# Kernel tuning notes

Hardware: AMD Instinct MI355X
Metric: run time of the kernel (lower is better)

## Reference

```python
import jax, jax.numpy as jnp
import numpy as np

QUALITY = 95
X_MIN, X_MAX = 0.0, 1.0

# JPEG Annex K base quantization tables
_LUMA = np.array([
    [16, 11, 10, 16, 24, 40, 51, 61],
    [12, 12, 14, 19, 26, 58, 60, 55],
    [14, 13, 16, 24, 40, 57, 69, 56],
    [14, 17, 22, 29, 51, 87, 80, 62],
    [18, 22, 37, 56, 68, 109, 103, 77],
    [24, 35, 55, 64, 81, 104, 113, 92],
    [49, 64, 78, 87, 103, 121, 120, 101],
    [72, 92, 95, 98, 112, 100, 103, 99]], dtype=np.float32)
_CHROMA = np.array([
    [17, 18, 24, 47, 99, 99, 99, 99],
    [18, 21, 26, 66, 99, 99, 99, 99],
    [24, 26, 56, 99, 99, 99, 99, 99],
    [47, 66, 99, 99, 99, 99, 99, 99],
    [99, 99, 99, 99, 99, 99, 99, 99],
    [99, 99, 99, 99, 99, 99, 99, 99],
    [99, 99, 99, 99, 99, 99, 99, 99],
    [99, 99, 99, 99, 99, 99, 99, 99]], dtype=np.float32)

def _qtable(base, quality):
    # libjpeg quality scaling (quality >= 50 branch)
    scale = 5000.0 / quality if quality < 50 else 200.0 - 2.0 * quality
    return np.clip(np.floor((base * scale + 50.0) / 100.0), 1.0, 255.0).astype(np.float32)

_QL = jnp.asarray(_qtable(_LUMA, QUALITY))
_QC = jnp.asarray(_qtable(_CHROMA, QUALITY))

# Orthonormal 8x8 DCT-II matrix
_k = np.arange(8)
_D = np.sqrt(2.0 / 8.0) * np.cos((2 * _k[None, :] + 1) * _k[:, None] * np.pi / 16.0)
_D[0, :] /= np.sqrt(2.0)
_D = jnp.asarray(_D.astype(np.float32))

def _jpeg_channel(ch, table):
    """8x8 block DCT -> quantize(round) -> dequantize -> IDCT. ch: [B,H,W] level-shifted."""
    B, H, W = ch.shape
    xb = ch.reshape(B, H // 8, 8, W // 8, 8)
    coef = jnp.einsum('ki,bhiwj,lj->bhkwl', _D, xb, _D)
    t = table[None, None, :, None, :]
    deq = jnp.round(coef / t) * t
    rec = jnp.einsum('ki,bhkwl,lj->bhiwj', _D, deq, _D)
    return rec.reshape(B, H, W)

def _jpeg_roundtrip(x255):
    """x255: [B,H,W,3] float values in [0,255]. Simulates JPEG encode+decode (4:2:0)."""
    r, g, b = x255[..., 0], x255[..., 1], x255[..., 2]
    # JFIF RGB -> YCbCr
    y = 0.299 * r + 0.587 * g + 0.114 * b
    cb = -0.168736 * r - 0.331264 * g + 0.5 * b + 128.0
    cr = 0.5 * r - 0.418688 * g - 0.081312 * b + 128.0
    # Luma at full resolution
    y2 = _jpeg_channel(y - 128.0, _QL) + 128.0
    # Chroma: 2x2 average downsample (4:2:0), codec, nearest upsample
    def down(c):
        B, H, W = c.shape
        return c.reshape(B, H // 2, 2, W // 2, 2).mean(axis=(2, 4))
    def up(c):
        return jnp.repeat(jnp.repeat(c, 2, axis=1), 2, axis=2)
    cb2 = up(_jpeg_channel(down(cb) - 128.0, _QC) + 128.0)
    cr2 = up(_jpeg_channel(down(cr) - 128.0, _QC) + 128.0)
    # YCbCr -> RGB
    r2 = y2 + 1.402 * (cr2 - 128.0)
    g2 = y2 - 0.344136 * (cb2 - 128.0) - 0.714136 * (cr2 - 128.0)
    b2 = y2 + 1.772 * (cb2 - 128.0)
    rgb = jnp.stack([r2, g2, b2], axis=-1)
    return jnp.round(jnp.clip(rgb, 0.0, 255.0))  # decoded uint8 values


def setup_inputs() -> dict:
    key = jax.random.key(0)
    x = jax.random.uniform(key, (32, 512, 512, 3), dtype=jnp.float32)
    return {"x": x}


def reference(x):
    # inputs -> uint8 pixel values (tf.cast truncation; values are >= 0)
    x255 = jnp.clip(jnp.floor((x - X_MIN) / ((X_MAX - X_MIN) / 255.0)), 0.0, 255.0)
    dec = _jpeg_roundtrip(x255)
    # back to input range/dtype
    return dec / (255.0 / (X_MAX - X_MIN)) + X_MIN
```

## Files before the change

kernel.cpp:

```cpp
#include <hip/hip_runtime.h>
#include <cstddef>

static constexpr float D8[8][8] = {
  { 0.35355339059327373f, 0.35355339059327373f, 0.35355339059327373f, 0.35355339059327373f,
    0.35355339059327373f, 0.35355339059327373f, 0.35355339059327373f, 0.35355339059327373f},
  { 0.4903926402016152f,  0.4157348061512726f,  0.27778511650980114f, 0.09754516100806417f,
   -0.09754516100806417f,-0.27778511650980114f,-0.4157348061512726f, -0.4903926402016152f},
  { 0.46193976625564337f, 0.19134171618254492f,-0.19134171618254492f,-0.46193976625564337f,
   -0.46193976625564337f,-0.19134171618254492f, 0.19134171618254492f, 0.46193976625564337f},
  { 0.4157348061512726f, -0.09754516100806417f,-0.4903926402016152f, -0.27778511650980114f,
    0.27778511650980114f, 0.4903926402016152f,  0.09754516100806417f,-0.4157348061512726f},
  { 0.35355339059327373f,-0.35355339059327373f,-0.35355339059327373f, 0.35355339059327373f,
    0.35355339059327373f,-0.35355339059327373f,-0.35355339059327373f, 0.35355339059327373f},
  { 0.27778511650980114f,-0.4903926402016152f,  0.09754516100806417f, 0.4157348061512726f,
   -0.4157348061512726f, -0.09754516100806417f, 0.4903926402016152f, -0.27778511650980114f},
  { 0.19134171618254492f,-0.46193976625564337f, 0.46193976625564337f,-0.19134171618254492f,
   -0.19134171618254492f, 0.46193976625564337f,-0.46193976625564337f, 0.19134171618254492f},
  { 0.09754516100806417f,-0.27778511650980114f, 0.4157348061512726f, -0.4903926402016152f,
    0.4903926402016152f, -0.4157348061512726f,  0.27778511650980114f,-0.09754516100806417f},
};

static constexpr float QLt[8][8] = {
  {2,1,1,2,2,4,5,6},
  {1,1,1,2,3,6,6,6},
  {1,1,2,2,4,6,7,6},
  {1,2,2,3,5,9,8,6},
  {2,2,4,6,7,11,10,8},
  {2,4,6,6,8,10,11,9},
  {5,6,8,9,10,12,12,10},
  {7,9,10,10,11,10,10,10},
};
static constexpr float QCt[8][8] = {
  {2,2,2,5,10,10,10,10},
  {2,2,3,7,10,10,10,10},
  {2,3,6,10,10,10,10,10},
  {5,7,10,10,10,10,10,10},
  {10,10,10,10,10,10,10,10},
  {10,10,10,10,10,10,10,10},
  {10,10,10,10,10,10,10,10},
  {10,10,10,10,10,10,10,10},
};

__device__ __forceinline__ void dct8(const float x[8], float u[8]) {
  #pragma unroll
  for (int k = 0; k < 8; ++k) {
    float a = D8[k][0] * x[0];
    #pragma unroll
    for (int j = 1; j < 8; ++j) a += D8[k][j] * x[j];
    u[k] = a;
  }
}

__device__ __forceinline__ void idct8(const float x[8], float u[8]) {
  #pragma unroll
  for (int j = 0; j < 8; ++j) {
    float a = x[0] * D8[0][j];
    #pragma unroll
    for (int m = 1; m < 8; ++m) a += x[m] * D8[m][j];
    u[j] = a;
  }
}

__global__ __launch_bounds__(256) void jpeg_rt(const float* __restrict__ in,
                                               float* __restrict__ out)
{
  __shared__ __align__(16) float Yp[16][132];
  __shared__ __align__(16) float Cbp[8][68];
  __shared__ __align__(16) float Crp[8][68];
  __shared__ __align__(16) float S1[32][72];
  __shared__ __align__(16) float S2[32][72];

  const int t   = threadIdx.x;
  const int tx  = blockIdx.x;
  const int ty  = blockIdx.y;
  const int img = blockIdx.z;

  const int pr = t >> 5;
  const int pc = t & 31;

  const float c255 = (float)(1.0/255.0);

  {
    float yv[2][4];
    float cbv[2][4], crv[2][4];
    #pragma unroll
    for (int rr = 0; rr < 2; ++rr) {
      const size_t grow = (size_t)img * 512 + (size_t)(ty*16 + 2*pr + rr);
      const float* rp = in + (grow*512 + (size_t)(tx*128 + 4*pc))*3;
      float4 A = ((const float4*)rp)[0];
      float4 Bq = ((const float4*)rp)[1];
      float4 Cq = ((const float4*)rp)[2];
      float px[12] = {A.x,A.y,A.z,A.w,Bq.x,Bq.y,Bq.z,Bq.w,Cq.x,Cq.y,Cq.z,Cq.w};
      #pragma unroll
      for (int p = 0; p < 4; ++p) {
        float r = fminf(fmaxf(floorf(px[3*p+0]/c255), 0.0f), 255.0f);
        float g = fminf(fmaxf(floorf(px[3*p+1]/c255), 0.0f), 255.0f);
        float b = fminf(fmaxf(floorf(px[3*p+2]/c255), 0.0f), 255.0f);
        float y  =  0.299f*r + 0.587f*g + 0.114f*b;
        float cb = -0.168736f*r - 0.331264f*g + 0.5f*b + 128.0f;
        float cr =  0.5f*r - 0.418688f*g - 0.081312f*b + 128.0f;
        yv[rr][p]  = y - 128.0f;
        cbv[rr][p] = cb;
        crv[rr][p] = cr;
      }
    }
    *(float4*)&Yp[2*pr+0][4*pc] = make_float4(yv[0][0],yv[0][1],yv[0][2],yv[0][3]);
    *(float4*)&Yp[2*pr+1][4*pc] = make_float4(yv[1][0],yv[1][1],yv[1][2],yv[1][3]);
    float cb0 = ((cbv[0][0]+cbv[0][1]) + (cbv[1][0]+cbv[1][1]))*0.25f - 128.0f;
    float cb1 = ((cbv[0][2]+cbv[0][3]) + (cbv[1][2]+cbv[1][3]))*0.25f - 128.0f;
    float cr0 = ((crv[0][0]+crv[0][1]) + (crv[1][0]+crv[1][1]))*0.25f - 128.0f;
    float cr1 = ((crv[0][2]+crv[0][3]) + (crv[1][2]+crv[1][3]))*0.25f - 128.0f;
    *(float2*)&Cbp[pr][2*pc] = make_float2(cb0, cb1);
    *(float2*)&Crp[pr][2*pc] = make_float2(cr0, cr1);
  }
  __syncthreads();

  {
    const int b = t >> 3, i = t & 7;
    const int br = b >> 4, bc = b & 15;
    const float* src = &Yp[br*8 + i][bc*8];
    float xr[8], u[8];
    *(float4*)&xr[0] = *(const float4*)&src[0];
    *(float4*)&xr[4] = *(const float4*)&src[4];
    dct8(xr, u);
    *(float4*)&S1[b][i*8+0] = make_float4(u[0],u[1],u[2],u[3]);
    *(float4*)&S1[b][i*8+4] = make_float4(u[4],u[5],u[6],u[7]);
  }
  __syncthreads();

  {
    const int b = t >> 3, kk = t & 7;
    float s[8], u[8], v[8];
    #pragma unroll
    for (int i = 0; i < 8; ++i) s[i] = S1[b][i*8 + kk];
    dct8(s, u);
    #pragma unroll
    for (int m = 0; m < 8; ++m) {
      float qv = QLt[m][kk];
      u[m] = rintf(u[m]/qv) * qv;
    }
    idct8(u, v);
    *(float4*)&S2[b][kk*8+0] = make_float4(v[0],v[1],v[2],v[3]);
    *(float4*)&S2[b][kk*8+4] = make_float4(v[4],v[5],v[6],v[7]);
  }
  __syncthreads();

  {
    const int b = t >> 3, j = t & 7;
    float w[8], z[8];
    #pragma unroll
    for (int m = 0; m < 8; ++m) w[m] = S2[b][m*8 + j];
    idct8(w, z);
    const int br = b >> 4, bc = b & 15;
    *(float4*)&Yp[br*8 + j][bc*8 + 0] = make_float4(z[0],z[1],z[2],z[3]);
    *(float4*)&Yp[br*8 + j][bc*8 + 4] = make_float4(z[4],z[5],z[6],z[7]);
  }
  if (t < 128) {
    const int b = t >> 3, i = t & 7;
    const float* plane = (b & 8) ? &Crp[0][0] : &Cbp[0][0];
    const float* src = plane + i*68 + (b & 7)*8;
    float xr[8], u[8];
    *(float4*)&xr[0] = *(const float4*)&src[0];
    *(float4*)&xr[4] = *(const float4*)&src[4];
    dct8(xr, u);
    *(float4*)&S1[b][i*8+0] = make_float4(u[0],u[1],u[2],u[3]);
    *(float4*)&S1[b][i*8+4] = make_float4(u[4],u[5],u[6],u[7]);
  }
  __syncthreads();

  if (t < 128) {
    const int b = t >> 3, kk = t & 7;
    float s[8], u[8], v[8];
    #pragma unroll
    for (int i = 0; i < 8; ++i) s[i] = S1[b][i*8 + kk];
    dct8(s, u);
    #pragma unroll
    for (int m = 0; m < 8; ++m) {
      float qv = QCt[m][kk];
      u[m] = rintf(u[m]/qv) * qv;
    }
    idct8(u, v);
    *(float4*)&S2[b][kk*8+0] = make_float4(v[0],v[1],v[2],v[3]);
    *(float4*)&S2[b][kk*8+4] = make_float4(v[4],v[5],v[6],v[7]);
  }
  __syncthreads();

  if (t < 128) {
    const int b = t >> 3, j = t & 7;
    float w[8], z[8];
    #pragma unroll
    for (int m = 0; m < 8; ++m) w[m] = S2[b][m*8 + j];
    idct8(w, z);
    float* plane = (b & 8) ? &Crp[0][0] : &Cbp[0][0];
    float* dst = plane + j*68 + (b & 7)*8;
    *(float4*)&dst[0] = make_float4(z[0],z[1],z[2],z[3]);
    *(float4*)&dst[4] = make_float4(z[4],z[5],z[6],z[7]);
  }
  __syncthreads();

  {
    float y0[4], y1[4];
    *(float4*)y0 = *(const float4*)&Yp[2*pr+0][4*pc];
    *(float4*)y1 = *(const float4*)&Yp[2*pr+1][4*pc];
    float2 cbp2 = *(const float2*)&Cbp[pr][2*pc];
    float2 crp2 = *(const float2*)&Crp[pr][2*pc];
    float cbq[2] = {cbp2.x, cbp2.y};
    float crq[2] = {crp2.x, crp2.y};
    #pragma unroll
    for (int rr = 0; rr < 2; ++rr) {
      float ov[12];
      #pragma unroll
      for (int p = 0; p < 4; ++p) {
        float y2  = (rr ? y1[p] : y0[p]) + 128.0f;
        float cb2 = cbq[p>>1] + 128.0f;
        float cr2 = crq[p>>1] + 128.0f;
        float r2 = y2 + 1.402f*(cr2 - 128.0f);
        float g2 = y2 - 0.344136f*(cb2 - 128.0f) - 0.714136f*(cr2 - 128.0f);
        float b2 = y2 + 1.772f*(cb2 - 128.0f);
        ov[3*p+0] = rintf(fminf(fmaxf(r2, 0.0f), 255.0f)) / 255.0f;
        ov[3*p+1] = rintf(fminf(fmaxf(g2, 0.0f), 255.0f)) / 255.0f;
        ov[3*p+2] = rintf(fminf(fmaxf(b2, 0.0f), 255.0f)) / 255.0f;
      }
      const size_t grow = (size_t)img * 512 + (size_t)(ty*16 + 2*pr + rr);
      float* op = out + (grow*512 + (size_t)(tx*128 + 4*pc))*3;
      ((float4*)op)[0] = make_float4(ov[0],ov[1],ov[2],ov[3]);
      ((float4*)op)[1] = make_float4(ov[4],ov[5],ov[6],ov[7]);
      ((float4*)op)[2] = make_float4(ov[8],ov[9],ov[10],ov[11]);
    }
  }
}

extern "C" void kernel_launch(void* const* d_in, const int* in_sizes, int n_in,
                              void* d_out, int out_size, void* d_ws, size_t ws_size,
                              hipStream_t stream) {
  (void)in_sizes; (void)n_in; (void)d_ws; (void)ws_size; (void)out_size;
  const float* x = (const float*)d_in[0];
  float* out = (float*)d_out;
  dim3 grid(4, 32, 32);
  jpeg_rt<<<grid, dim3(256), 0, stream>>>(x, out);
}
```

Measured before the change: 182.0 us.

## Transpose DCT blocks with lane shuffles and replace divisions with reciprocal-FMA

Each 8x8 block is now handled by 8 lanes that do the row DCT, transpose through __shfl_xor butterflies, do the column DCT, quantize, and invert, all in registers. This removes the S1/S2 shared-memory staging and four __syncthreads barriers. Divisions by 1/255, by 255 and by the quantization steps become a multiply by the reciprocal plus one FMA correction, using reciprocals precomputed in a small shared table. The shuffle transpose costs extra cross-lane instructions, and the correction step may not reproduce IEEE division exactly in every case.

```diff
diff --git a/kernel.cpp b/kernel.cpp
--- a/kernel.cpp
+++ b/kernel.cpp
@@ -41,6 +41,15 @@
   {10,10,10,10,10,10,10,10},
 };
 
+static constexpr float C255  = (float)(1.0/255.0);
+static constexpr float RC255 = 1.0f / C255;
+
+__device__ __forceinline__ float exact_div(float x, float c, float r) {
+  float q0 = x * r;
+  float e  = fmaf(-c, q0, x);
+  return fmaf(e, r, q0);
+}
+
 __device__ __forceinline__ void dct8(const float x[8], float u[8]) {
   #pragma unroll
   for (int k = 0; k < 8; ++k) {
@@ -58,6 +67,21 @@
     #pragma unroll
     for (int m = 1; m < 8; ++m) a += x[m] * D8[m][j];
     u[j] = a;
+  }
+}
+
+__device__ __forceinline__ void xpose8(float v[8], int lane) {
+  #pragma unroll
+  for (int s = 1; s < 8; s <<= 1) {
+    const bool hi = (lane & s) != 0;
+    #pragma unroll
+    for (int r0 = 0; r0 < 8; ++r0) {
+      if (r0 & s) continue;
+      const int r1 = r0 | s;
+      float send = hi ? v[r0] : v[r1];
+      float got  = __shfl_xor(send, s, 64);
+      if (hi) v[r0] = got; else v[r1] = got;
+    }
   }
 }
 
@@ -67,8 +91,8 @@
   __shared__ __align__(16) float Yp[16][132];
   __shared__ __align__(16) float Cbp[8][68];
   __shared__ __align__(16) float Crp[8][68];
-  __shared__ __align__(16) float S1[32][72];
-  __shared__ __align__(16) float S2[32][72];
+  __shared__ __align__(16) float QTs[2][8][8];
+  __shared__ __align__(16) float RQs[2][8][8];
 
   const int t   = threadIdx.x;
   const int tx  = blockIdx.x;
@@ -78,7 +102,12 @@
   const int pr = t >> 5;
   const int pc = t & 31;
 
-  const float c255 = (float)(1.0/255.0);
+  if (t < 128) {
+    const int pl = t >> 6, i = (t >> 3) & 7, m = t & 7;
+    const float q = pl ? QCt[m][i] : QLt[m][i];
+    QTs[pl][i][m] = q;
+    RQs[pl][i][m] = 1.0f / q;
+  }
 
   {
     float yv[2][4];
@@ -93,9 +122,9 @@
       float px[12] = {A.x,A.y,A.z,A.w,Bq.x,Bq.y,Bq.z,Bq.w,Cq.x,Cq.y,Cq.z,Cq.w};
       #pragma unroll
       for (int p = 0; p < 4; ++p) {
-        float r = fminf(fmaxf(floorf(px[3*p+0]/c255), 0.0f), 255.0f);
-        float g = fminf(fmaxf(floorf(px[3*p+1]/c255), 0.0f), 255.0f);
-        float b = fminf(fmaxf(floorf(px[3*p+2]/c255), 0.0f), 255.0f);
+        float r = fminf(fmaxf(floorf(exact_div(px[3*p+0], C255, RC255)), 0.0f), 255.0f);
+        float g = fminf(fmaxf(floorf(exact_div(px[3*p+1], C255, RC255)), 0.0f), 255.0f);
+        float b = fminf(fmaxf(floorf(exact_div(px[3*p+2], C255, RC255)), 0.0f), 255.0f);
         float y  =  0.299f*r + 0.587f*g + 0.114f*b;
         float cb = -0.168736f*r - 0.331264f*g + 0.5f*b + 128.0f;
         float cr =  0.5f*r - 0.418688f*g - 0.081312f*b + 128.0f;
@@ -116,85 +145,52 @@
   __syncthreads();
 
   {
-    const int b = t >> 3, i = t & 7;
-    const int br = b >> 4, bc = b & 15;
-    const float* src = &Yp[br*8 + i][bc*8];
-    float xr[8], u[8];
-    *(float4*)&xr[0] = *(const float4*)&src[0];
-    *(float4*)&xr[4] = *(const float4*)&src[4];
-    dct8(xr, u);
-    *(float4*)&S1[b][i*8+0] = make_float4(u[0],u[1],u[2],u[3]);
-    *(float4*)&S1[b][i*8+4] = make_float4(u[4],u[5],u[6],u[7]);
-  }
-  __syncthreads();
-
-  {
-    const int b = t >> 3, kk = t & 7;
-    float s[8], u[8], v[8];
-    #pragma unroll
-    for (int i = 0; i < 8; ++i) s[i] = S1[b][i*8 + kk];
-    dct8(s, u);
-    #pragma unroll
-    for (int m = 0; m < 8; ++m) {
-      float qv = QLt[m][kk];
-      u[m] = rintf(u[m]/qv) * qv;
-    }
+    const int g = t >> 3, l = t & 7;
+    const int br = g >> 4, bc = g & 15;
+    float* rowp = &Yp[br*8 + l][bc*8];
+    float v[8], u[8];
+    *(float4*)&v[0] = *(const float4*)&rowp[0];
+    *(float4*)&v[4] = *(const float4*)&rowp[4];
+    dct8(v, u);
+    xpose8(u, l);
+    dct8(u, v);
+    float qv[8], rv[8];
+    *(float4*)&qv[0] = *(const float4*)&QTs[0][l][0];
+    *(float4*)&qv[4] = *(const float4*)&QTs[0][l][4];
+    *(float4*)&rv[0] = *(const float4*)&RQs[0][l][0];
+    *(float4*)&rv[4] = *(const float4*)&RQs[0][l][4];
+    #pragma unroll
+    for (int m = 0; m < 8; ++m)
+      v[m] = rintf(exact_div(v[m], qv[m], rv[m])) * qv[m];
+    idct8(v, u);
+    xpose8(u, l);
     idct8(u, v);
-    *(float4*)&S2[b][kk*8+0] = make_float4(v[0],v[1],v[2],v[3]);
-    *(float4*)&S2[b][kk*8+4] = make_float4(v[4],v[5],v[6],v[7]);
-  }
-  __syncthreads();
-
-  {
-    const int b = t >> 3, j = t & 7;
-    float w[8], z[8];
-    #pragma unroll
-    for (int m = 0; m < 8; ++m) w[m] = S2[b][m*8 + j];
-    idct8(w, z);
-    const int br = b >> 4, bc = b & 15;
-    *(float4*)&Yp[br*8 + j][bc*8 + 0] = make_float4(z[0],z[1],z[2],z[3]);
-    *(float4*)&Yp[br*8 + j][bc*8 + 4] = make_float4(z[4],z[5],z[6],z[7]);
+    *(float4*)&rowp[0] = *(float4*)&v[0];
+    *(float4*)&rowp[4] = *(float4*)&v[4];
   }
   if (t < 128) {
-    const int b = t >> 3, i = t & 7;
-    const float* plane = (b & 8) ? &Crp[0][0] : &Cbp[0][0];
-    const float* src = plane + i*68 + (b & 7)*8;
-    float xr[8], u[8];
-    *(float4*)&xr[0] = *(const float4*)&src[0];
-    *(float4*)&xr[4] = *(const float4*)&src[4];
-    dct8(xr, u);
-    *(float4*)&S1[b][i*8+0] = make_float4(u[0],u[1],u[2],u[3]);
-    *(float4*)&S1[b][i*8+4] = make_float4(u[4],u[5],u[6],u[7]);
-  }
-  __syncthreads();
-
-  if (t < 128) {
-    const int b = t >> 3, kk = t & 7;
-    float s[8], u[8], v[8];
-    #pragma unroll
-    for (int i = 0; i < 8; ++i) s[i] = S1[b][i*8 + kk];
-    dct8(s, u);
-    #pragma unroll
-    for (int m = 0; m < 8; ++m) {
-      float qv = QCt[m][kk];
-      u[m] = rintf(u[m]/qv) * qv;
-    }
+    const int g = t >> 3, l = t & 7;
+    float* plane = (g & 8) ? &Crp[0][0] : &Cbp[0][0];
+    float* rowp = plane + l*68 + (g & 7)*8;
+    float v[8], u[8];
+    *(float4*)&v[0] = *(const float4*)&rowp[0];
+    *(float4*)&v[4] = *(const float4*)&rowp[4];
+    dct8(v, u);
+    xpose8(u, l);
+    dct8(u, v);
+    float qv[8], rv[8];
+    *(float4*)&qv[0] = *(const float4*)&QTs[1][l][0];
+    *(float4*)&qv[4] = *(const float4*)&QTs[1][l][4];
+    *(float4*)&rv[0] = *(const float4*)&RQs[1][l][0];
+    *(float4*)&rv[4] = *(const float4*)&RQs[1][l][4];
+    #pragma unroll
+    for (int m = 0; m < 8; ++m)
+      v[m] = rintf(exact_div(v[m], qv[m], rv[m])) * qv[m];
+    idct8(v, u);
+    xpose8(u, l);
     idct8(u, v);
-    *(float4*)&S2[b][kk*8+0] = make_float4(v[0],v[1],v[2],v[3]);
-    *(float4*)&S2[b][kk*8+4] = make_float4(v[4],v[5],v[6],v[7]);
-  }
-  __syncthreads();
-
-  if (t < 128) {
-    const int b = t >> 3, j = t & 7;
-    float w[8], z[8];
-    #pragma unroll
-    for (int m = 0; m < 8; ++m) w[m] = S2[b][m*8 + j];
-    idct8(w, z);
-    float* plane = (b & 8) ? &Crp[0][0] : &Cbp[0][0];
-    float* dst = plane + j*68 + (b & 7)*8;
-    *(float4*)&dst[0] = make_float4(z[0],z[1],z[2],z[3]);
-    *(float4*)&dst[4] = make_float4(z[4],z[5],z[6],z[7]);
+    *(float4*)&rowp[0] = *(float4*)&v[0];
+    *(float4*)&rowp[4] = *(float4*)&v[4];
   }
   __syncthreads();
 
@@ -217,9 +213,9 @@
         float r2 = y2 + 1.402f*(cr2 - 128.0f);
         float g2 = y2 - 0.344136f*(cb2 - 128.0f) - 0.714136f*(cr2 - 128.0f);
         float b2 = y2 + 1.772f*(cb2 - 128.0f);
-        ov[3*p+0] = rintf(fminf(fmaxf(r2, 0.0f), 255.0f)) / 255.0f;
-        ov[3*p+1] = rintf(fminf(fmaxf(g2, 0.0f), 255.0f)) / 255.0f;
-        ov[3*p+2] = rintf(fminf(fmaxf(b2, 0.0f), 255.0f)) / 255.0f;
+        ov[3*p+0] = exact_div(rintf(fminf(fmaxf(r2, 0.0f), 255.0f)), 255.0f, C255);
+        ov[3*p+1] = exact_div(rintf(fminf(fmaxf(g2, 0.0f), 255.0f)), 255.0f, C255);
+        ov[3*p+2] = exact_div(rintf(fminf(fmaxf(b2, 0.0f), 255.0f)), 255.0f, C255);
       }
       const size_t grow = (size_t)img * 512 + (size_t)(ty*16 + 2*pr + rr);
       float* op = out + (grow*512 + (size_t)(tx*128 + 4*pc))*3;
```

New measurement: 223.3 us. 1.23x slower.
